# Performance work log

Hardware: AMD Instinct MI355X
Metric: run time of the kernel (lower is better)

Reference implementation:

```python
import jax, jax.numpy as jnp
import numpy as np

BS = 32  # leaf block size
NUM_HOPS = 1  # ATTENTION_HOPS


def setup_inputs() -> dict:
    key = jax.random.key(0)
    ks = jax.random.split(key, 10)
    B, N, C, H = 1, 131072, 256, 4
    E = 8 * N
    x = jax.random.normal(ks[0], (B, N, C), dtype=jnp.float32)
    rows = jax.random.randint(ks[1], (E,), 0, N)
    offs = jax.random.randint(ks[2], (E,), 0, BS)
    cols = (rows // BS) * BS + offs  # in-block neighbors
    edge_index = jnp.stack([rows, cols]).astype(jnp.int64)
    edge_values = jax.random.normal(ks[3], (E,), dtype=jnp.float32)
    positions = jax.random.uniform(ks[4], (N, 3), dtype=jnp.float32)
    qkv_w = jax.random.normal(ks[5], (3 * C, C), dtype=jnp.float32) * 0.02
    qkv_b = jnp.zeros((3 * C,), dtype=jnp.float32)
    proj_w = jax.random.normal(ks[6], (C, C), dtype=jnp.float32) * 0.02
    proj_b = jnp.zeros((C,), dtype=jnp.float32)
    gate_w = jax.random.normal(ks[7], (H, 4), dtype=jnp.float32) * 0.01  # init std=0.01
    gate_b = jnp.zeros((H,), dtype=jnp.float32)
    return {"x": x, "edge_index": edge_index, "edge_values": edge_values,
            "positions": positions, "qkv_w": qkv_w, "qkv_b": qkv_b,
            "proj_w": proj_w, "proj_b": proj_b, "gate_w": gate_w, "gate_b": gate_b}


def _connectivity(edge_index, edge_values, positions, nb):
    rows, cols = edge_index[0], edge_index[1]
    br, bc = rows // BS, cols // BS
    in_block = (br == bc) & (br < nb)
    r_l, c_l = rows % BS, cols % BS
    b_safe = jnp.where(in_block, br, nb)  # out-of-range -> dropped by scatter
    dx = positions[cols] - positions[rows]            # [E,3]
    ef_flat = jnp.concatenate([dx, edge_values[:, None]], axis=1)  # [E,4]
    adj = jnp.zeros((nb, BS, BS), jnp.float32).at[b_safe, r_l, c_l].set(1.0, mode='drop')
    eye = jnp.eye(BS, dtype=jnp.float32)
    reachable = jnp.broadcast_to(eye[None], (nb, BS, BS))
    cur = adj
    for _ in range(NUM_HOPS):
        reachable = jnp.clip(reachable + cur, 0.0, 1.0)
        cur = jnp.matmul(cur, adj)
    attn_mask = jnp.concatenate([reachable, jnp.ones((nb, BS, 1), jnp.float32)], axis=2)
    edge_feats = jnp.zeros((nb, BS, BS + 1, 4), jnp.float32)
    edge_feats = edge_feats.at[b_safe, r_l, c_l, :].set(ef_flat, mode='drop')
    return attn_mask, edge_feats


def reference(x, edge_index, edge_values, positions, qkv_w, qkv_b, proj_w, proj_b, gate_w, gate_b):
    B, N, C = x.shape
    H = gate_w.shape[0]
    hd = C // H
    scale = hd ** -0.5
    nb = N // BS  # N chosen divisible by BS (no pad)
    attn_mask, edge_feats = _connectivity(edge_index, edge_values, positions, nb)

    x_blk = x.reshape(B, nb, BS, C)
    block_node = x_blk.mean(axis=2, keepdims=True)
    kv = jnp.concatenate([x_blk, block_node], axis=2)  # [B,nb,BS+1,C]
    qkv_q = x_blk @ qkv_w.T + qkv_b
    qkv_kv = kv @ qkv_w.T + qkv_b
    q = qkv_q[..., :C].reshape(B, nb, BS, H, hd)
    k = qkv_kv[..., C:2 * C].reshape(B, nb, BS + 1, H, hd)
    v = qkv_kv[..., 2 * C:].reshape(B, nb, BS + 1, H, hd)

    scores = jnp.einsum('bnqhd,bnkhd->bnqkh', q, k) * scale

    ar = jnp.arange(BS)
    bias_physics = edge_feats.at[:, :, BS, :].set(0.0).at[:, :, BS, 3].set(1.0)
    bias_physics = bias_physics.at[:, ar, ar, :].set(0.0).at[:, ar, ar, 3].set(1.0)

    scores = scores + bias_physics[None, ..., 3:4]
    mask = attn_mask[None, :, :, :, None]  # [1,nb,BS,BS+1,1]
    scores = jnp.where(mask == 0, -jnp.inf, scores)
    attn_probs = jax.nn.softmax(scores, axis=3)

    gate = bias_physics @ gate_w.T + gate_b  # [nb,BS,BS+1,H]
    gate = jnp.where(mask == 0, 0.0, gate[None])
    combined = attn_probs + gate

    x_out = jnp.einsum('bnqkh,bnkhd->bnqhd', combined, v).reshape(B, nb, BS, C)
    out = x_out.reshape(B, N, C) @ proj_w.T + proj_b
    return out
```

## Files before the change

### kernel.cpp

```cpp
#include <hip/hip_runtime.h>
#include <math.h>

#define BSZ 32
#define CH  256

typedef short  bf16x8 __attribute__((ext_vector_type(8)));
typedef float  f32x4  __attribute__((ext_vector_type(4)));
typedef unsigned short ushort_t;
typedef unsigned int   uint_t;

#define MFMA(a, b, c) __builtin_amdgcn_mfma_f32_16x16x32_bf16((a), (b), (c), 0, 0, 0)

__device__ __forceinline__ ushort_t f2b(float f) {
    uint_t u = __builtin_bit_cast(uint_t, f);
    uint_t r = (u + 0x7FFFu + ((u >> 16) & 1u)) >> 16;
    return (ushort_t)r;
}
__device__ __forceinline__ float b2f(ushort_t u) {
    uint_t v = ((uint_t)u) << 16;
    return __builtin_bit_cast(float, v);
}
__device__ __forceinline__ uint_t pk2(float a, float b) {
    return (uint_t)f2b(a) | ((uint_t)f2b(b) << 16);
}
__device__ __forceinline__ bf16x8 u4b8(uint4 u) {
    return __builtin_bit_cast(bf16x8, u);
}

__global__ void edge_win_kernel(const int* __restrict__ ei, int E, int nb,
                                int* __restrict__ win) {
    int e = blockIdx.x * blockDim.x + threadIdx.x;
    if (e >= E) return;
    int r = ei[e];
    int c = ei[E + e];
    int br = r >> 5, bc = c >> 5;
    if (br == bc && br < nb) {
        atomicMax(&win[br * (BSZ * BSZ) + (r & 31) * BSZ + (c & 31)], e);
    }
}

__global__ void edge_feat_kernel(const int* __restrict__ ei,
                                 const float* __restrict__ ev,
                                 const float* __restrict__ pos,
                                 const int* __restrict__ win, int E,
                                 ushort_t* __restrict__ cellinfo) {
    int e = blockIdx.x * blockDim.x + threadIdx.x;
    if (e >= E) return;
    int r = ei[e];
    int c = ei[E + e];
    int br = r >> 5, bc = c >> 5;
    if (br != bc) return;
    int cell = br * 1024 + (r & 31) * 32 + (c & 31);
    if (win[cell] != e) return;
    float d0 = pos[c * 3 + 0] - pos[r * 3 + 0];
    float d1 = pos[c * 3 + 1] - pos[r * 3 + 1];
    float d2 = pos[c * 3 + 2] - pos[r * 3 + 2];
    float d3 = ev[e];
    uint2 w; w.x = pk2(d0, d1); w.y = pk2(d2, d3);
    *(uint2*)&cellinfo[(size_t)cell * 4] = w;
}

__global__ void wconv_kernel(const float* __restrict__ qkv_w,
                             const float* __restrict__ proj_w,
                             ushort_t* __restrict__ qkv_wf,
                             ushort_t* __restrict__ proj_wf) {
    int i = blockIdx.x * blockDim.x + threadIdx.x;
    int lane = i & 63, ks = (i >> 6) & 7, tile = i >> 9;
    int l15 = lane & 15, lg = lane >> 4;
    if (tile < 48) {
        const float* src = qkv_w + (size_t)(tile * 16 + l15) * 256 + ks * 32 + lg * 8;
        ushort_t* dst = qkv_wf + (size_t)i * 8;
        #pragma unroll
        for (int e = 0; e < 8; ++e) dst[e] = f2b(src[e]);
    }
    if (tile < 16) {
        const float* src = proj_w + (size_t)(tile * 16 + l15) * 256 + ks * 32 + lg * 8;
        ushort_t* dst = proj_wf + (size_t)i * 8;
        #pragma unroll
        for (int e = 0; e < 8; ++e) dst[e] = f2b(src[e]);
    }
}

#define LS_XB   0
#define LS_QS   32768
#define LS_KS   65536
#define LS_VS   98304
#define LS_TOT  131072

__global__ __launch_bounds__(512, 2)
void fused_attn(const float* __restrict__ x,
                const ushort_t* __restrict__ qkv_wf,
                const float* __restrict__ qkv_b,
                const ushort_t* __restrict__ cellinfo,
                const ushort_t* __restrict__ proj_wf,
                const float* __restrict__ proj_b,
                const float* __restrict__ gate_w,
                const float* __restrict__ gate_b,
                float* __restrict__ out)
{
    __shared__ __align__(16) char smem[LS_TOT];
    ushort_t* xb   = (ushort_t*)(smem + LS_XB);
    ushort_t* comb = (ushort_t*)(smem + LS_XB);
    ushort_t* qs   = (ushort_t*)(smem + LS_QS);
    ushort_t* xo   = (ushort_t*)(smem + LS_QS);
    ushort_t* ksm  = (ushort_t*)(smem + LS_KS);
    ushort_t* vs   = (ushort_t*)(smem + LS_VS);

    const int t = threadIdx.x;
    const int w = t >> 6, lane = t & 63, l15 = lane & 15, lg = lane >> 4;
    const int bi = blockIdx.x;
    const int mbase = bi * 64;

    #pragma unroll
    for (int i = 0; i < 8; ++i) {
        int flat = i * 2048 + t * 4;
        int r = flat >> 8, c = flat & 255;
        float4 xv = *(const float4*)&x[(size_t)(mbase + r) * CH + c];
        uint2 wv; wv.x = pk2(xv.x, xv.y); wv.y = pk2(xv.z, xv.w);
        *(uint2*)&xb[r * 256 + (c ^ ((r & 7) << 3))] = wv;
    }
    __syncthreads();

    const int slB = (l15 & 7) << 3;
    f32x4 acc[6][4];
    #pragma unroll
    for (int it = 0; it < 6; ++it)
        #pragma unroll
        for (int m = 0; m < 4; ++m) acc[it][m] = (f32x4){0.f, 0.f, 0.f, 0.f};

    bf16x8 xfA[4], xfB[4], wfA[6], wfB[6];

#define LOADX(dst, kss) { int k0_ = ((kss) * 32 + lg * 8) ^ slB;              \
        dst[0] = *(const bf16x8*)&xb[l15 * 256 + k0_];                        \
        dst[1] = *(const bf16x8*)&xb[(16 + l15) * 256 + k0_];                 \
        dst[2] = *(const bf16x8*)&xb[(32 + l15) * 256 + k0_];                 \
        dst[3] = *(const bf16x8*)&xb[(48 + l15) * 256 + k0_]; }

#define LOADW(dst, kss) { _Pragma("unroll")                                   \
        for (int it_ = 0; it_ < 6; ++it_)                                     \
            dst[it_] = *(const bf16x8*)(qkv_wf                                \
                + ((size_t)(((it_ * 8 + w) * 8) + (kss))) * 512 + lane * 8); }

#define COMPUTE(xf, wf) { _Pragma("unroll")                                   \
        for (int it_ = 0; it_ < 6; ++it_) {                                   \
            if (it_ < 4) { _Pragma("unroll")                                  \
                for (int m_ = 0; m_ < 4; ++m_)                                \
                    acc[it_][m_] = MFMA(wf[it_], xf[m_], acc[it_][m_]);       \
            } else { _Pragma("unroll")                                        \
                for (int m_ = 0; m_ < 4; ++m_)                                \
                    acc[it_][m_] = MFMA(xf[m_], wf[it_], acc[it_][m_]); } } }

    LOADX(xfA, 0); LOADW(wfA, 0);
    LOADX(xfB, 1); LOADW(wfB, 1);
    COMPUTE(xfA, wfA);
    LOADX(xfA, 2); LOADW(wfA, 2);
    COMPUTE(xfB, wfB);
    LOADX(xfB, 3); LOADW(wfB, 3);
    COMPUTE(xfA, wfA);
    LOADX(xfA, 4); LOADW(wfA, 4);
    COMPUTE(xfB, wfB);
    LOADX(xfB, 5); LOADW(wfB, 5);
    COMPUTE(xfA, wfA);
    LOADX(xfA, 6); LOADW(wfA, 6);
    COMPUTE(xfB, wfB);
    LOADX(xfB, 7); LOADW(wfB, 7);
    COMPUTE(xfA, wfA);
    COMPUTE(xfB, wfB);

    #pragma unroll
    for (int it = 0; it < 6; ++it) {
        int tt = it * 8 + w;
        if (it < 4) {
            f32x4 bv4 = *(const f32x4*)&qkv_b[tt * 16 + lg * 4];
            ushort_t* dst = (it < 2) ? qs : ksm;
            int tloc = (it < 2) ? tt : tt - 16;
            #pragma unroll
            for (int m = 0; m < 4; ++m) {
                f32x4 v = acc[it][m] + bv4;
                uint2 wv; wv.x = pk2(v[0], v[1]); wv.y = pk2(v[2], v[3]);
                int g = m >> 1;
                *(uint2*)&dst[g * 8192 + (tloc * 2 + (m & 1)) * 256 + lane * 4] = wv;
            }
        } else {
            int vch = (tt - 32) * 16 + l15;
            float bv = qkv_b[512 + vch];
            int swzv = (vch & 3) << 3;
            #pragma unroll
            for (int m = 0; m < 4; ++m) {
                f32x4 v = acc[it][m];
                uint2 wv; wv.x = pk2(v[0] + bv, v[1] + bv);
                wv.y = pk2(v[2] + bv, v[3] + bv);
                int g = m >> 1;
                int roff = ((m & 1) * 16 + lg * 4) ^ swzv;
                *(uint2*)&vs[g * 8192 + vch * 32 + roff] = wv;
            }
        }
    }

    const int gl = w >> 2, h = w & 3;
    const ushort_t* crow = cellinfo + (size_t)(bi * 2 + gl) * 4096;
    uint4 cellA[2][2], cellB[2][2];
    #pragma unroll
    for (int qt = 0; qt < 2; ++qt) {
        int qi = qt * 16 + l15;
        #pragma unroll
        for (int kt = 0; kt < 2; ++kt) {
            int kj0 = kt * 16 + lg * 4;
            const uint_t* cp = (const uint_t*)(crow + ((size_t)qi * 32 + kj0) * 4);
            cellA[qt][kt] = *(const uint4*)cp;
            cellB[qt][kt] = *(const uint4*)(cp + 4);
        }
    }
    const float gw0 = gate_w[h * 4 + 0], gw1 = gate_w[h * 4 + 1];
    const float gw2 = gate_w[h * 4 + 2], gw3 = gate_w[h * 4 + 3];
    const float gb  = gate_b[h];

    __syncthreads();

    uint4 qld[2][2], kld[2][2];
    #pragma unroll
    for (int rt = 0; rt < 2; ++rt) {
        #pragma unroll
        for (int ks2 = 0; ks2 < 2; ++ks2) {
            int ttq = h * 4 + ks2 * 2 + (lg >> 1);
            int a0 = gl * 8192 + (ttq * 2 + rt) * 256 + ((lg & 1) * 32 + l15) * 4;
            uint2 u0 = *(const uint2*)&qs[a0];
            uint2 u1 = *(const uint2*)&qs[a0 + 64];
            qld[rt][ks2] = (uint4){u0.x, u0.y, u1.x, u1.y};
            uint2 w0 = *(const uint2*)&ksm[a0];
            uint2 w1 = *(const uint2*)&ksm[a0 + 64];
            kld[rt][ks2] = (uint4){w0.x, w0.y, w1.x, w1.y};
        }
    }
    bf16x8 vf[4];
    #pragma unroll
    for (int ct = 0; ct < 4; ++ct) {
        int off = (lg * 8) ^ ((l15 & 3) << 3);
        vf[ct] = *(const bf16x8*)&vs[gl * 8192
                                     + (h * 64 + ct * 16 + l15) * 32 + off];
    }
    __syncthreads();

    f32x4 s[2][2];
    #pragma unroll
    for (int qt = 0; qt < 2; ++qt) {
        s[qt][0] = (f32x4){0.f, 0.f, 0.f, 0.f};
        s[qt][1] = (f32x4){0.f, 0.f, 0.f, 0.f};
    }
    #pragma unroll
    for (int qt = 0; qt < 2; ++qt) {
        #pragma unroll
        for (int ks2 = 0; ks2 < 2; ++ks2) {
            bf16x8 qf = u4b8(qld[qt][ks2]);
            #pragma unroll
            for (int kt = 0; kt < 2; ++kt)
                s[qt][kt] = MFMA(u4b8(kld[kt][ks2]), qf, s[qt][kt]);
        }
    }

    #pragma unroll
    for (int qt = 0; qt < 2; ++qt) {
        int qi = qt * 16 + l15;
        float r[8], gt[8];
        float rawsum = 0.f;
        #pragma unroll
        for (int kt = 0; kt < 2; ++kt) {
            int kj0 = kt * 16 + lg * 4;
            uint4 cA = cellA[qt][kt], cB = cellB[qt][kt];
            uint_t d01[4] = {cA.x, cA.z, cB.x, cB.z};
            uint_t d23[4] = {cA.y, cA.w, cB.y, cB.w};
            #pragma unroll
            for (int j = 0; j < 4; ++j) {
                int kj = kj0 + j;
                bool fixed = (kj == qi);
                ushort_t e3b = (ushort_t)(d23[j] >> 16);
                bool valid = (e3b != (ushort_t)0xFFFFu);
                float e3 = b2f(e3b);
                float sb = fixed ? 1.0f : (valid ? e3 : -INFINITY);
                float g;
                if (fixed)      g = gw3 + gb;
                else if (valid) g = b2f((ushort_t)(d01[j] & 0xFFFF)) * gw0
                                  + b2f((ushort_t)(d01[j] >> 16))    * gw1
                                  + b2f((ushort_t)(d23[j] & 0xFFFF)) * gw2
                                  + e3 * gw3 + gb;
                else            g = 0.0f;
                float sraw = s[qt][kt][j];
                rawsum += sraw;
                r[kt * 4 + j]  = sraw * 0.125f + sb;
                gt[kt * 4 + j] = g;
            }
        }
        rawsum += __shfl_xor(rawsum, 16);
        rawsum += __shfl_xor(rawsum, 32);
        float r2 = rawsum * (0.125f / 32.0f) + 1.0f;

        float m = fmaxf(fmaxf(fmaxf(r[0], r[1]), fmaxf(r[2], r[3])),
                        fmaxf(fmaxf(r[4], r[5]), fmaxf(r[6], r[7])));
        m = fmaxf(m, r2);
        m = fmaxf(m, __shfl_xor(m, 16));
        m = fmaxf(m, __shfl_xor(m, 32));
        float sum = 0.f;
        #pragma unroll
        for (int i = 0; i < 8; ++i) { r[i] = __expf(r[i] - m); sum += r[i]; }
        sum += __shfl_xor(sum, 16);
        sum += __shfl_xor(sum, 32);
        float e2 = __expf(r2 - m);
        float inv = 1.0f / (sum + e2);
        float comb32 = e2 * inv + (gw3 + gb);
        float cadd = comb32 * 0.03125f;
        int swz = (l15 & 3) << 3;
        #pragma unroll
        for (int kt = 0; kt < 2; ++kt) {
            int kj0 = kt * 16 + lg * 4;
            uint2 wv;
            wv.x = pk2(r[kt*4+0] * inv + gt[kt*4+0] + cadd,
                       r[kt*4+1] * inv + gt[kt*4+1] + cadd);
            wv.y = pk2(r[kt*4+2] * inv + gt[kt*4+2] + cadd,
                       r[kt*4+3] * inv + gt[kt*4+3] + cadd);
            *(uint2*)&comb[(gl * 4 + h) * 1024 + qi * 32 + (kj0 ^ swz)] = wv;
        }
    }

    bf16x8 cfr[2];
    #pragma unroll
    for (int qt = 0; qt < 2; ++qt) {
        int qi = qt * 16 + l15;
        int off = (lg * 8) ^ ((l15 & 3) << 3);
        cfr[qt] = *(const bf16x8*)&comb[(gl * 4 + h) * 1024 + qi * 32 + off];
    }
    #pragma unroll
    for (int ct = 0; ct < 4; ++ct) {
        #pragma unroll
        for (int qt = 0; qt < 2; ++qt) {
            f32x4 acc2 = {0.f, 0.f, 0.f, 0.f};
            acc2 = MFMA(vf[ct], cfr[qt], acc2);
            int qi = qt * 16 + l15;
            uint2 wv;
            wv.x = pk2(acc2[0], acc2[1]);
            wv.y = pk2(acc2[2], acc2[3]);
            int c0 = h * 64 + ct * 16 + lg * 4;
            *(uint2*)&xo[gl * 8192 + qi * 256 + (c0 ^ ((l15 & 7) << 3))] = wv;
        }
    }
    __syncthreads();

    {
        const int slR = (l15 & 7) << 3;
        bf16x8 pw[2][8];
        #pragma unroll
        for (int i = 0; i < 2; ++i) {
            int pt = w * 2 + i;
            #pragma unroll
            for (int ks = 0; ks < 8; ++ks)
                pw[i][ks] = *(const bf16x8*)(proj_wf
                               + ((size_t)(pt * 8 + ks)) * 512 + lane * 8);
        }
        f32x4 pacc[2][4];
        #pragma unroll
        for (int i = 0; i < 2; ++i)
            #pragma unroll
            for (int rt = 0; rt < 4; ++rt) pacc[i][rt] = (f32x4){0.f,0.f,0.f,0.f};
        #pragma unroll
        for (int ks = 0; ks < 8; ++ks) {
            int k0 = ks * 32 + lg * 8;
            #pragma unroll
            for (int rt = 0; rt < 4; ++rt) {
                bf16x8 bfr = *(const bf16x8*)&xo[(rt >> 1) * 8192
                                 + ((rt & 1) * 16 + l15) * 256 + (k0 ^ slR)];
                pacc[0][rt] = MFMA(pw[0][ks], bfr, pacc[0][rt]);
                pacc[1][rt] = MFMA(pw[1][ks], bfr, pacc[1][rt]);
            }
        }
        #pragma unroll
        for (int i = 0; i < 2; ++i) {
            int pt = w * 2 + i, n0 = pt * 16;
            f32x4 bv = *(const f32x4*)&proj_b[n0 + lg * 4];
            #pragma unroll
            for (int rt = 0; rt < 4; ++rt) {
                f32x4 o = pacc[i][rt] + bv;
                int row = mbase + (rt >> 1) * 32 + (rt & 1) * 16 + l15;
                *(f32x4*)&out[(size_t)row * 256 + n0 + lg * 4] = o;
            }
        }
    }
}

extern "C" void kernel_launch(void* const* d_in, const int* in_sizes, int n_in,
                              void* d_out, int out_size, void* d_ws, size_t ws_size,
                              hipStream_t stream) {
    const float* x      = (const float*)d_in[0];
    const int*   ei     = (const int*)  d_in[1];
    const float* ev     = (const float*)d_in[2];
    const float* pos    = (const float*)d_in[3];
    const float* qkv_w  = (const float*)d_in[4];
    const float* qkv_b  = (const float*)d_in[5];
    const float* proj_w = (const float*)d_in[6];
    const float* proj_b = (const float*)d_in[7];
    const float* gate_w = (const float*)d_in[8];
    const float* gate_b = (const float*)d_in[9];
    float* out = (float*)d_out;

    const int E  = in_sizes[2];
    const int N  = in_sizes[0] / CH;
    const int nb = N / BSZ;

    char* ws = (char*)d_ws;
    int*      win      = (int*)ws;
    ushort_t* cellinfo = (ushort_t*)(ws + (size_t)nb * 4096);
    size_t off = (size_t)nb * 12288;
    ushort_t* qkv_wf  = (ushort_t*)(ws + off); off += 48 * 8 * 64 * 8 * 2;
    ushort_t* proj_wf = (ushort_t*)(ws + off); off += 16 * 8 * 64 * 8 * 2;

    hipMemsetAsync(ws, 0xFF, (size_t)nb * 12288, stream);
    edge_win_kernel<<<(E + 255) / 256, 256, 0, stream>>>(ei, E, nb, win);
    edge_feat_kernel<<<(E + 255) / 256, 256, 0, stream>>>(ei, ev, pos, win, E,
                                                          cellinfo);
    wconv_kernel<<<96, 256, 0, stream>>>(qkv_w, proj_w, qkv_wf, proj_wf);
    fused_attn<<<nb / 2, 512, 0, stream>>>(x, qkv_wf, qkv_b, cellinfo,
                                           proj_wf, proj_b, gate_w, gate_b, out);
}
```

Measured before the change: 262.8 us.

## Add validity bitmap to skip cellinfo memset and restructure QKV GEMM per tile

Adds a per-row 32-bit validity bitmap, built with atomicOr in the edge feature kernel, so the 8 KB-per-block cellinfo array no longer needs a 0xFF memset. The attention kernel reads the mask from the bitmap rather than from a sentinel value. The QKV projection is reordered to keep all x fragments in registers and compute one output tile at a time, with double-buffered weight loads. This cuts memset traffic and accumulator register pressure, but raises the register count for x fragments and adds atomics.

```diff
diff --git a/kernel.cpp b/kernel.cpp
--- a/kernel.cpp
+++ b/kernel.cpp
@@ -22,9 +22,6 @@
 }
 __device__ __forceinline__ uint_t pk2(float a, float b) {
     return (uint_t)f2b(a) | ((uint_t)f2b(b) << 16);
-}
-__device__ __forceinline__ bf16x8 u4b8(uint4 u) {
-    return __builtin_bit_cast(bf16x8, u);
 }
 
 __global__ void edge_win_kernel(const int* __restrict__ ei, int E, int nb,
@@ -43,14 +40,16 @@
                                  const float* __restrict__ ev,
                                  const float* __restrict__ pos,
                                  const int* __restrict__ win, int E,
-                                 ushort_t* __restrict__ cellinfo) {
+                                 ushort_t* __restrict__ cellinfo,
+                                 uint_t* __restrict__ vmap) {
     int e = blockIdx.x * blockDim.x + threadIdx.x;
     if (e >= E) return;
     int r = ei[e];
     int c = ei[E + e];
     int br = r >> 5, bc = c >> 5;
     if (br != bc) return;
-    int cell = br * 1024 + (r & 31) * 32 + (c & 31);
+    int rl = r & 31, cl = c & 31;
+    int cell = br * 1024 + rl * 32 + cl;
     if (win[cell] != e) return;
     float d0 = pos[c * 3 + 0] - pos[r * 3 + 0];
     float d1 = pos[c * 3 + 1] - pos[r * 3 + 1];
@@ -58,6 +57,7 @@
     float d3 = ev[e];
     uint2 w; w.x = pk2(d0, d1); w.y = pk2(d2, d3);
     *(uint2*)&cellinfo[(size_t)cell * 4] = w;
+    atomicOr(&vmap[br * 32 + rl], 1u << cl);
 }
 
 __global__ void wconv_kernel(const float* __restrict__ qkv_w,
@@ -92,6 +92,7 @@
                 const ushort_t* __restrict__ qkv_wf,
                 const float* __restrict__ qkv_b,
                 const ushort_t* __restrict__ cellinfo,
+                const uint_t* __restrict__ vmap,
                 const ushort_t* __restrict__ proj_wf,
                 const float* __restrict__ proj_b,
                 const float* __restrict__ gate_w,
@@ -122,87 +123,89 @@
     __syncthreads();
 
     const int slB = (l15 & 7) << 3;
-    f32x4 acc[6][4];
-    #pragma unroll
-    for (int it = 0; it < 6; ++it)
-        #pragma unroll
-        for (int m = 0; m < 4; ++m) acc[it][m] = (f32x4){0.f, 0.f, 0.f, 0.f};
-
-    bf16x8 xfA[4], xfB[4], wfA[6], wfB[6];
-
-#define LOADX(dst, kss) { int k0_ = ((kss) * 32 + lg * 8) ^ slB;              \
-        dst[0] = *(const bf16x8*)&xb[l15 * 256 + k0_];                        \
-        dst[1] = *(const bf16x8*)&xb[(16 + l15) * 256 + k0_];                 \
-        dst[2] = *(const bf16x8*)&xb[(32 + l15) * 256 + k0_];                 \
-        dst[3] = *(const bf16x8*)&xb[(48 + l15) * 256 + k0_]; }
-
-#define LOADW(dst, kss) { _Pragma("unroll")                                   \
-        for (int it_ = 0; it_ < 6; ++it_)                                     \
-            dst[it_] = *(const bf16x8*)(qkv_wf                                \
-                + ((size_t)(((it_ * 8 + w) * 8) + (kss))) * 512 + lane * 8); }
-
-#define COMPUTE(xf, wf) { _Pragma("unroll")                                   \
-        for (int it_ = 0; it_ < 6; ++it_) {                                   \
-            if (it_ < 4) { _Pragma("unroll")                                  \
-                for (int m_ = 0; m_ < 4; ++m_)                                \
-                    acc[it_][m_] = MFMA(wf[it_], xf[m_], acc[it_][m_]);       \
-            } else { _Pragma("unroll")                                        \
-                for (int m_ = 0; m_ < 4; ++m_)                                \
-                    acc[it_][m_] = MFMA(xf[m_], wf[it_], acc[it_][m_]); } } }
-
-    LOADX(xfA, 0); LOADW(wfA, 0);
-    LOADX(xfB, 1); LOADW(wfB, 1);
-    COMPUTE(xfA, wfA);
-    LOADX(xfA, 2); LOADW(wfA, 2);
-    COMPUTE(xfB, wfB);
-    LOADX(xfB, 3); LOADW(wfB, 3);
-    COMPUTE(xfA, wfA);
-    LOADX(xfA, 4); LOADW(wfA, 4);
-    COMPUTE(xfB, wfB);
-    LOADX(xfB, 5); LOADW(wfB, 5);
-    COMPUTE(xfA, wfA);
-    LOADX(xfA, 6); LOADW(wfA, 6);
-    COMPUTE(xfB, wfB);
-    LOADX(xfB, 7); LOADW(wfB, 7);
-    COMPUTE(xfA, wfA);
-    COMPUTE(xfB, wfB);
-
-    #pragma unroll
-    for (int it = 0; it < 6; ++it) {
-        int tt = it * 8 + w;
-        if (it < 4) {
-            f32x4 bv4 = *(const f32x4*)&qkv_b[tt * 16 + lg * 4];
-            ushort_t* dst = (it < 2) ? qs : ksm;
-            int tloc = (it < 2) ? tt : tt - 16;
-            #pragma unroll
-            for (int m = 0; m < 4; ++m) {
-                f32x4 v = acc[it][m] + bv4;
-                uint2 wv; wv.x = pk2(v[0], v[1]); wv.y = pk2(v[2], v[3]);
-                int g = m >> 1;
-                *(uint2*)&dst[g * 8192 + (tloc * 2 + (m & 1)) * 256 + lane * 4] = wv;
-            }
-        } else {
-            int vch = (tt - 32) * 16 + l15;
-            float bv = qkv_b[512 + vch];
-            int swzv = (vch & 3) << 3;
-            #pragma unroll
-            for (int m = 0; m < 4; ++m) {
-                f32x4 v = acc[it][m];
-                uint2 wv; wv.x = pk2(v[0] + bv, v[1] + bv);
-                wv.y = pk2(v[2] + bv, v[3] + bv);
-                int g = m >> 1;
-                int roff = ((m & 1) * 16 + lg * 4) ^ swzv;
-                *(uint2*)&vs[g * 8192 + vch * 32 + roff] = wv;
-            }
-        }
-    }
+    const f32x4 zf = {0.f, 0.f, 0.f, 0.f};
+
+    bf16x8 xf[8][4];
+    #pragma unroll
+    for (int ks = 0; ks < 8; ++ks) {
+        int k0 = (ks * 32 + lg * 8) ^ slB;
+        xf[ks][0] = *(const bf16x8*)&xb[l15 * 256 + k0];
+        xf[ks][1] = *(const bf16x8*)&xb[(16 + l15) * 256 + k0];
+        xf[ks][2] = *(const bf16x8*)&xb[(32 + l15) * 256 + k0];
+        xf[ks][3] = *(const bf16x8*)&xb[(48 + l15) * 256 + k0];
+    }
+
+    bf16x8 wA[8], wB[8];
+
+#define LOADT(dst, itv) { _Pragma("unroll")                                   \
+        for (int ks_ = 0; ks_ < 8; ++ks_)                                     \
+            dst[ks_] = *(const bf16x8*)(qkv_wf                                \
+                + ((size_t)((((itv) * 8 + w) * 8) + ks_)) * 512 + lane * 8); }
+
+#define TILE_COMPUTE(CUR, SW) { _Pragma("unroll")                             \
+        for (int ks_ = 0; ks_ < 8; ++ks_) {                                   \
+            if (SW) {                                                         \
+                a0 = MFMA(CUR[ks_], xf[ks_][0], a0);                          \
+                a1 = MFMA(CUR[ks_], xf[ks_][1], a1);                          \
+                a2 = MFMA(CUR[ks_], xf[ks_][2], a2);                          \
+                a3 = MFMA(CUR[ks_], xf[ks_][3], a3);                          \
+            } else {                                                          \
+                a0 = MFMA(xf[ks_][0], CUR[ks_], a0);                          \
+                a1 = MFMA(xf[ks_][1], CUR[ks_], a1);                          \
+                a2 = MFMA(xf[ks_][2], CUR[ks_], a2);                          \
+                a3 = MFMA(xf[ks_][3], CUR[ks_], a3);                          \
+            } } }
+
+#define STORE_QK(ITV) {                                                       \
+        int tt_ = (ITV) * 8 + w;                                              \
+        f32x4 bv4_ = *(const f32x4*)&qkv_b[tt_ * 16 + lg * 4];                \
+        ushort_t* dst_ = ((ITV) < 2) ? qs : ksm;                              \
+        int tloc_ = ((ITV) < 2) ? tt_ : tt_ - 16;                             \
+        f32x4 av_[4] = {a0, a1, a2, a3};                                      \
+        _Pragma("unroll")                                                     \
+        for (int m_ = 0; m_ < 4; ++m_) {                                      \
+            f32x4 v_ = av_[m_] + bv4_;                                        \
+            uint2 wv_; wv_.x = pk2(v_[0], v_[1]); wv_.y = pk2(v_[2], v_[3]);  \
+            *(uint2*)&dst_[(m_ >> 1) * 8192 + (tloc_ * 2 + (m_ & 1)) * 256    \
+                           + lane * 4] = wv_;                                 \
+        } }
+
+#define STORE_V(ITV) {                                                        \
+        int tt_ = (ITV) * 8 + w;                                              \
+        int vch_ = (tt_ - 32) * 16 + l15;                                     \
+        float bv_ = qkv_b[512 + vch_];                                        \
+        int swzv_ = (vch_ & 3) << 3;                                          \
+        f32x4 av_[4] = {a0, a1, a2, a3};                                      \
+        _Pragma("unroll")                                                     \
+        for (int m_ = 0; m_ < 4; ++m_) {                                      \
+            f32x4 v_ = av_[m_];                                               \
+            uint2 wv_; wv_.x = pk2(v_[0] + bv_, v_[1] + bv_);                 \
+            wv_.y = pk2(v_[2] + bv_, v_[3] + bv_);                            \
+            int roff_ = (((m_ & 1) * 16 + lg * 4)) ^ swzv_;                   \
+            *(uint2*)&vs[(m_ >> 1) * 8192 + vch_ * 32 + roff_] = wv_;         \
+        } }
+
+#define DO_TILE(ITV, CUR) {                                                   \
+        f32x4 a0 = zf, a1 = zf, a2 = zf, a3 = zf;                             \
+        if ((ITV) < 4) { TILE_COMPUTE(CUR, 1) STORE_QK(ITV) }                 \
+        else           { TILE_COMPUTE(CUR, 0) STORE_V(ITV) } }
+
+    LOADT(wA, 0); LOADT(wB, 1);
+    DO_TILE(0, wA); LOADT(wA, 2);
+    DO_TILE(1, wB); LOADT(wB, 3);
+    DO_TILE(2, wA); LOADT(wA, 4);
+    DO_TILE(3, wB); LOADT(wB, 5);
+    DO_TILE(4, wA);
+    DO_TILE(5, wB);
 
     const int gl = w >> 2, h = w & 3;
     const ushort_t* crow = cellinfo + (size_t)(bi * 2 + gl) * 4096;
     uint4 cellA[2][2], cellB[2][2];
+    uint_t vmq[2];
     #pragma unroll
     for (int qt = 0; qt < 2; ++qt) {
         int qi = qt * 16 + l15;
+        vmq[qt] = vmap[(size_t)(bi * 2 + gl) * 32 + qi];
         #pragma unroll
         for (int kt = 0; kt < 2; ++kt) {
             int kj0 = kt * 16 + lg * 4;
@@ -243,18 +246,16 @@
 
     f32x4 s[2][2];
     #pragma unroll
+    for (int qt = 0; qt < 2; ++qt) { s[qt][0] = zf; s[qt][1] = zf; }
+    #pragma unroll
     for (int qt = 0; qt < 2; ++qt) {
-        s[qt][0] = (f32x4){0.f, 0.f, 0.f, 0.f};
-        s[qt][1] = (f32x4){0.f, 0.f, 0.f, 0.f};
-    }
-    #pragma unroll
-    for (int qt = 0; qt < 2; ++qt) {
         #pragma unroll
         for (int ks2 = 0; ks2 < 2; ++ks2) {
-            bf16x8 qf = u4b8(qld[qt][ks2]);
+            bf16x8 qf = __builtin_bit_cast(bf16x8, qld[qt][ks2]);
             #pragma unroll
             for (int kt = 0; kt < 2; ++kt)
-                s[qt][kt] = MFMA(u4b8(kld[kt][ks2]), qf, s[qt][kt]);
+                s[qt][kt] = MFMA(__builtin_bit_cast(bf16x8, kld[kt][ks2]),
+                                 qf, s[qt][kt]);
         }
     }
 
@@ -273,17 +274,16 @@
             for (int j = 0; j < 4; ++j) {
                 int kj = kj0 + j;
                 bool fixed = (kj == qi);
-                ushort_t e3b = (ushort_t)(d23[j] >> 16);
-                bool valid = (e3b != (ushort_t)0xFFFFu);
-                float e3 = b2f(e3b);
-                float sb = fixed ? 1.0f : (valid ? e3 : -INFINITY);
+                bool validb = (vmq[qt] >> kj) & 1u;
+                float e3 = b2f((ushort_t)(d23[j] >> 16));
+                float sb = fixed ? 1.0f : (validb ? e3 : -INFINITY);
                 float g;
-                if (fixed)      g = gw3 + gb;
-                else if (valid) g = b2f((ushort_t)(d01[j] & 0xFFFF)) * gw0
-                                  + b2f((ushort_t)(d01[j] >> 16))    * gw1
-                                  + b2f((ushort_t)(d23[j] & 0xFFFF)) * gw2
-                                  + e3 * gw3 + gb;
-                else            g = 0.0f;
+                if (fixed)       g = gw3 + gb;
+                else if (validb) g = b2f((ushort_t)(d01[j] & 0xFFFF)) * gw0
+                                   + b2f((ushort_t)(d01[j] >> 16))    * gw1
+                                   + b2f((ushort_t)(d23[j] & 0xFFFF)) * gw2
+                                   + e3 * gw3 + gb;
+                else             g = 0.0f;
                 float sraw = s[qt][kt][j];
                 rawsum += sraw;
                 r[kt * 4 + j]  = sraw * 0.125f + sb;
@@ -332,7 +332,7 @@
     for (int ct = 0; ct < 4; ++ct) {
         #pragma unroll
         for (int qt = 0; qt < 2; ++qt) {
-            f32x4 acc2 = {0.f, 0.f, 0.f, 0.f};
+            f32x4 acc2 = zf;
             acc2 = MFMA(vf[ct], cfr[qt], acc2);
             int qi = qt * 16 + l15;
             uint2 wv;
@@ -359,7 +359,7 @@
         #pragma unroll
         for (int i = 0; i < 2; ++i)
             #pragma unroll
-            for (int rt = 0; rt < 4; ++rt) pacc[i][rt] = (f32x4){0.f,0.f,0.f,0.f};
+            for (int rt = 0; rt < 4; ++rt) pacc[i][rt] = zf;
         #pragma unroll
         for (int ks = 0; ks < 8; ++ks) {
             int k0 = ks * 32 + lg * 8;
@@ -406,16 +406,18 @@
 
     char* ws = (char*)d_ws;
     int*      win      = (int*)ws;
-    ushort_t* cellinfo = (ushort_t*)(ws + (size_t)nb * 4096);
-    size_t off = (size_t)nb * 12288;
+    uint_t*   vmap     = (uint_t*)(ws + (size_t)nb * 4096);
+    ushort_t* cellinfo = (ushort_t*)(ws + (size_t)nb * 4224);
+    size_t off = (size_t)nb * 12416;
     ushort_t* qkv_wf  = (ushort_t*)(ws + off); off += 48 * 8 * 64 * 8 * 2;
     ushort_t* proj_wf = (ushort_t*)(ws + off); off += 16 * 8 * 64 * 8 * 2;
 
-    hipMemsetAsync(ws, 0xFF, (size_t)nb * 12288, stream);
+    hipMemsetAsync(win, 0xFF, (size_t)nb * 4096, stream);
+    hipMemsetAsync(vmap, 0x00, (size_t)nb * 128, stream);
     edge_win_kernel<<<(E + 255) / 256, 256, 0, stream>>>(ei, E, nb, win);
     edge_feat_kernel<<<(E + 255) / 256, 256, 0, stream>>>(ei, ev, pos, win, E,
-                                                          cellinfo);
+                                                          cellinfo, vmap);
     wconv_kernel<<<96, 256, 0, stream>>>(qkv_w, proj_w, qkv_wf, proj_wf);
-    fused_attn<<<nb / 2, 512, 0, stream>>>(x, qkv_wf, qkv_b, cellinfo,
+    fused_attn<<<nb / 2, 512, 0, stream>>>(x, qkv_wf, qkv_b, cellinfo, vmap,
                                            proj_wf, proj_b, gate_w, gate_b, out);
 }
```

New measurement: 269.6 us. 2.6% more time.
